# Performance work log

Measured on AMD Instinct MI355X. Metric: run time of the kernel, lower is better.

## Reference

```python
import jax, jax.numpy as jnp
import numpy as np

T, D, FF, E, R = 4096, 1024, 2048, 4, 16
LORA_SCALE = 32.0 / 16.0  # alpha / r


def setup_inputs() -> dict:
    key = jax.random.key(0)
    ks = jax.random.split(key, 12)
    return {
        "x": jax.random.normal(ks[0], (T, D), jnp.float32),
        "gate_w": jax.random.normal(ks[1], (E, D), jnp.float32) * 0.03,
        "gate_up_w": jax.random.normal(ks[2], (D, 2 * FF), jnp.float32)[None].repeat(E, 0) * 0.0
                     + jax.random.normal(ks[2], (E, D, 2 * FF), jnp.float32) * 0.03,
        "gate_up_b": jax.random.normal(ks[3], (E, 2 * FF), jnp.float32) * 0.01,
        "down_w": jax.random.normal(ks[4], (E, FF, D), jnp.float32) * 0.02,
        "down_b": jax.random.normal(ks[5], (E, D), jnp.float32) * 0.01,
        "A_gate": jax.random.normal(ks[6], (E, R, D), jnp.float32) * 0.02,
        "B_gate": jax.random.normal(ks[7], (E, FF, R), jnp.float32) * 0.02,
        "A_up": jax.random.normal(ks[8], (E, R, D), jnp.float32) * 0.02,
        "B_up": jax.random.normal(ks[9], (E, FF, R), jnp.float32) * 0.02,
        "A_down": jax.random.normal(ks[10], (E, R, FF), jnp.float32) * 0.02,
        "B_down": jax.random.normal(ks[11], (E, D, R), jnp.float32) * 0.02,
        "top_k": 2,
    }


def reference(x, gate_w, gate_up_w, gate_up_b, down_w, down_b,
              A_gate, B_gate, A_up, B_up, A_down, B_down, top_k):
    t, d = x.shape
    e = gate_w.shape[0]
    # --- router: logits, softmax (fp32), top-k, renormalize ---
    router_logits = x @ gate_w.T                                   # [T,E]
    rw = jax.nn.softmax(router_logits.astype(jnp.float32), axis=1)
    top_w, sel = jax.lax.top_k(rw, top_k)                          # [T,k]
    top_w = top_w / jnp.sum(top_w, axis=-1, keepdims=True)
    top_w = top_w.astype(x.dtype)
    # dense per-token per-expert combine weights (scatter of top-k weights)
    w = jnp.zeros((t, e), x.dtype).at[jnp.arange(t)[:, None], sel].add(top_w)  # [T,E]
    # --- per-expert SwiGLU MLP with LoRA (vectorized over experts) ---
    gu = jnp.einsum('td,edf->etf', x, gate_up_w) + gate_up_b[:, None, :]       # [E,T,2FF]
    ff = gu.shape[-1] // 2
    gate = gu[..., :ff] + jnp.einsum('td,erd,efr->etf', x, A_gate, B_gate) * LORA_SCALE
    up = gu[..., ff:] + jnp.einsum('td,erd,efr->etf', x, A_up, B_up) * LORA_SCALE
    act = jax.nn.silu(gate) * up                                               # [E,T,FF]
    down = jnp.einsum('etf,efd->etd', act, down_w) + down_b[:, None, :]
    down = down + jnp.einsum('etf,erf,edr->etd', act, A_down, B_down) * LORA_SCALE
    # --- weighted scatter-combine ---
    final = jnp.einsum('etd,te->td', down, w)                                  # [T,D]
    return final, router_logits
```

## Files before the change

kernel.cpp:

```cpp
#include <hip/hip_runtime.h>

#define T_TOK 4096
#define DIM   1024
#define FFD   2048
#define NEXP  4
#define NRP   8704
#define MTILES 68

typedef unsigned short u16;
typedef __attribute__((ext_vector_type(8))) short short8;
typedef __attribute__((ext_vector_type(4))) float f32x4;
typedef __attribute__((ext_vector_type(8))) unsigned short u16x8;
typedef __attribute__((ext_vector_type(4))) unsigned short u16x4;

typedef __attribute__((address_space(1))) unsigned int as1_u32;
typedef __attribute__((address_space(3))) unsigned int as3_u32;

__device__ __forceinline__ u16 f2bf(float f) {
  union { float f; unsigned u; } v; v.f = f;
  unsigned u = v.u;
  return (u16)((u + 0x7fffu + ((u >> 16) & 1u)) >> 16);
}
__device__ __forceinline__ float bf2f(u16 h) {
  union { unsigned u; float f; } v; v.u = ((unsigned)h) << 16;
  return v.f;
}
__device__ __forceinline__ void gload16(const void* g, void* l) {
  __builtin_amdgcn_global_load_lds((const as1_u32*)g, (as3_u32*)l, 16, 0, 0);
}

__global__ void router_k(const float* __restrict__ x, const float* __restrict__ gw,
                         float* __restrict__ logits_out, int* __restrict__ sel,
                         float* __restrict__ selw) {
  int t = blockIdx.x;
  int lane = threadIdx.x;
  float xv[16];
#pragma unroll
  for (int i = 0; i < 16; ++i) xv[i] = x[(size_t)t * DIM + lane + i * 64];
  float l[4];
#pragma unroll
  for (int e = 0; e < 4; ++e) {
    float s = 0.f;
#pragma unroll
    for (int i = 0; i < 16; ++i) s += xv[i] * gw[e * DIM + lane + i * 64];
#pragma unroll
    for (int off = 32; off > 0; off >>= 1) s += __shfl_xor(s, off, 64);
    l[e] = s;
  }
  if (lane == 0) {
#pragma unroll
    for (int e = 0; e < 4; ++e) logits_out[(size_t)t * 4 + e] = l[e];
    int e0 = 0; float b0 = l[0];
    for (int e = 1; e < 4; ++e) if (l[e] > b0) { b0 = l[e]; e0 = e; }
    int e1 = -1; float b1 = -3.4e38f;
    for (int e = 0; e < 4; ++e) if (e != e0 && l[e] > b1) { b1 = l[e]; e1 = e; }
    float p1 = expf(b1 - b0);
    float w0 = 1.f / (1.f + p1);
    sel[2 * t] = e0; sel[2 * t + 1] = e1;
    selw[2 * t] = w0; selw[2 * t + 1] = 1.f - w0;
  }
}

__global__ void scan_k(const int* __restrict__ sel, int* __restrict__ pos,
                       int* __restrict__ offs, int* __restrict__ rowtok,
                       int* __restrict__ pairrow) {
  __shared__ int base[4];
  __shared__ int wsum[16][4];
  __shared__ int off_s[5];
  int tid = threadIdx.x, lane = tid & 63, wid = tid >> 6;
  if (tid < 4) base[tid] = 0;
  __syncthreads();
  for (int chunk = 0; chunk < 4; ++chunk) {
    int t = chunk * 1024 + tid;
    int e0 = sel[2 * t], e1 = sel[2 * t + 1];
    unsigned long long ltm = (1ull << lane) - 1ull;
    bool f[4]; int within[4];
#pragma unroll
    for (int e = 0; e < 4; ++e) {
      f[e] = (e0 == e) || (e1 == e);
      unsigned long long m = __ballot(f[e]);
      within[e] = __popcll(m & ltm);
      if (lane == 0) wsum[wid][e] = __popcll(m);
    }
    __syncthreads();
    int wbase[4] = {0, 0, 0, 0}, tot[4] = {0, 0, 0, 0};
    for (int i = 0; i < 16; ++i)
#pragma unroll
      for (int e = 0; e < 4; ++e) {
        int v = wsum[i][e];
        if (i < wid) wbase[e] += v;
        tot[e] += v;
      }
#pragma unroll
    for (int e = 0; e < 4; ++e)
      if (f[e]) {
        int p = base[e] + wbase[e] + within[e];
        if (e0 == e) pos[2 * t] = p; else pos[2 * t + 1] = p;
      }
    __syncthreads();
    if (tid < 4) base[tid] += tot[tid];
    __syncthreads();
  }
  if (tid == 0) {
    int o = 0;
    for (int e = 0; e < 4; ++e) { off_s[e] = o; o += ((base[e] + 127) >> 7) << 7; }
    off_s[4] = o;
    for (int i = 0; i < 5; ++i) offs[i] = off_s[i];
  }
  __syncthreads();
  for (int r = tid; r < NRP; r += 1024) rowtok[r] = -1;
  __syncthreads();
  for (int t = tid; t < T_TOK; t += 1024) {
#pragma unroll
    for (int s = 0; s < 2; ++s) {
      int e = sel[2 * t + s];
      int rr = off_s[e] + pos[2 * t + s];
      pairrow[2 * t + s] = rr;
      rowtok[rr] = t;
    }
  }
}

__global__ void gather_k(const float* __restrict__ x, const int* __restrict__ rowtok,
                         u16* __restrict__ xg) {
  int r = blockIdx.x, tid = threadIdx.x;
  int t = rowtok[r];
  float4 v = make_float4(0.f, 0.f, 0.f, 0.f);
  if (t >= 0) v = ((const float4*)(x + (size_t)t * DIM))[tid];
  u16x4 o;
  o[0] = f2bf(v.x); o[1] = f2bf(v.y); o[2] = f2bf(v.z); o[3] = f2bf(v.w);
  ((u16x4*)(xg + (size_t)r * DIM))[tid] = o;
}

__global__ void cvtA_k(const float* __restrict__ Ag, const float* __restrict__ Au,
                       const float* __restrict__ Ad, u16* __restrict__ abgu,
                       u16* __restrict__ adb) {
  int g = blockIdx.x * 256 + threadIdx.x;
  if (g < 32768) {
    int flat = g * 4;
    int e = flat >> 15;
    int rem = flat & 32767;
    int q = rem >> 10;
    int d = rem & 1023;
    const float* src = (q < 16) ? (Ag + ((size_t)e * 16 + q) * DIM + d)
                                : (Au + ((size_t)e * 16 + (q - 16)) * DIM + d);
    float4 v = *(const float4*)src;
    u16x4 o; o[0] = f2bf(v.x); o[1] = f2bf(v.y); o[2] = f2bf(v.z); o[3] = f2bf(v.w);
    *(u16x4*)(abgu + (size_t)flat) = o;
  } else {
    int flat = (g - 32768) * 4;
    float4 v = *(const float4*)(Ad + flat);
    u16x4 o; o[0] = f2bf(v.x); o[1] = f2bf(v.y); o[2] = f2bf(v.z); o[3] = f2bf(v.w);
    *(u16x4*)(adb + (size_t)flat) = o;
  }
}

__global__ void xa_k(const u16* __restrict__ xg, const u16* __restrict__ abgu,
                     const int* __restrict__ offs, float* __restrict__ xagu) {
  int r0 = blockIdx.x * 2, lane = threadIdx.x;
  int e = 0;
  if (r0 >= offs[1]) e = 1;
  if (r0 >= offs[2]) e = 2;
  if (r0 >= offs[3]) e = 3;
  float x0[16], x1[16];
#pragma unroll
  for (int i = 0; i < 4; ++i) {
    u16x4 v0 = ((const u16x4*)(xg + (size_t)r0 * DIM))[lane + i * 64];
    u16x4 v1 = ((const u16x4*)(xg + (size_t)(r0 + 1) * DIM))[lane + i * 64];
#pragma unroll
    for (int j = 0; j < 4; ++j) { x0[i * 4 + j] = bf2f(v0[j]); x1[i * 4 + j] = bf2f(v1[j]); }
  }
  const u16* A = abgu + (size_t)e * 32 * DIM;
  for (int q = 0; q < 32; ++q) {
    float s0 = 0.f, s1 = 0.f;
#pragma unroll
    for (int i = 0; i < 4; ++i) {
      u16x4 av = ((const u16x4*)(A + (size_t)q * DIM))[lane + i * 64];
#pragma unroll
      for (int j = 0; j < 4; ++j) {
        float a = bf2f(av[j]);
        s0 += x0[i * 4 + j] * a; s1 += x1[i * 4 + j] * a;
      }
    }
#pragma unroll
    for (int off = 32; off > 0; off >>= 1) { s0 += __shfl_xor(s0, off, 64); s1 += __shfl_xor(s1, off, 64); }
    if (lane == 0) { xagu[(size_t)r0 * 32 + q] = s0; xagu[(size_t)(r0 + 1) * 32 + q] = s1; }
  }
}

__global__ void aad_k(const u16* __restrict__ act, const u16* __restrict__ adb,
                      const int* __restrict__ offs, float* __restrict__ aad) {
  int r0 = blockIdx.x * 2, lane = threadIdx.x;
  int e = 0;
  if (r0 >= offs[1]) e = 1;
  if (r0 >= offs[2]) e = 2;
  if (r0 >= offs[3]) e = 3;
  float x0[32], x1[32];
#pragma unroll
  for (int i = 0; i < 8; ++i) {
    u16x4 v0 = ((const u16x4*)(act + (size_t)r0 * FFD))[lane + i * 64];
    u16x4 v1 = ((const u16x4*)(act + (size_t)(r0 + 1) * FFD))[lane + i * 64];
#pragma unroll
    for (int j = 0; j < 4; ++j) { x0[i * 4 + j] = bf2f(v0[j]); x1[i * 4 + j] = bf2f(v1[j]); }
  }
  const u16* A = adb + (size_t)e * 16 * FFD;
  for (int q = 0; q < 16; ++q) {
    float s0 = 0.f, s1 = 0.f;
#pragma unroll
    for (int i = 0; i < 8; ++i) {
      u16x4 av = ((const u16x4*)(A + (size_t)q * FFD))[lane + i * 64];
#pragma unroll
      for (int j = 0; j < 4; ++j) {
        float a = bf2f(av[j]);
        s0 += x0[i * 4 + j] * a; s1 += x1[i * 4 + j] * a;
      }
    }
#pragma unroll
    for (int off = 32; off > 0; off >>= 1) { s0 += __shfl_xor(s0, off, 64); s1 += __shfl_xor(s1, off, 64); }
    if (lane == 0) { aad[(size_t)r0 * 16 + q] = s0; aad[(size_t)(r0 + 1) * 16 + q] = s1; }
  }
}

__global__ void transpose_k(const float* __restrict__ in, u16* __restrict__ out,
                            int K, int N) {
  int e = blockIdx.z;
  int n0 = blockIdx.x * 32, k0 = blockIdx.y * 32;
  const float* I = in + (size_t)e * K * N;
  u16* O = out + (size_t)e * N * K;
  __shared__ u16 tile[32][33];
#pragma unroll
  for (int i = 0; i < 4; ++i) {
    int k = k0 + threadIdx.y + i * 8;
    tile[threadIdx.y + i * 8][threadIdx.x] = f2bf(I[(size_t)k * N + n0 + threadIdx.x]);
  }
  __syncthreads();
#pragma unroll
  for (int i = 0; i < 4; ++i) {
    int n = n0 + threadIdx.y + i * 8;
    O[(size_t)n * K + k0 + threadIdx.x] = tile[threadIdx.x][threadIdx.y + i * 8];
  }
}

__global__ __launch_bounds__(256) void gemm1_k(
    const u16* __restrict__ xg, const u16* __restrict__ wgu_t,
    const float* __restrict__ gub, const float* __restrict__ Bg,
    const float* __restrict__ Bu, const float* __restrict__ xagu,
    const int* __restrict__ offs, u16* __restrict__ act) {
  __shared__ __align__(16) u16 sAB[24576];
  int tid = threadIdx.x, w = tid >> 6, lane = tid & 63;
  int f0 = blockIdx.x * 64;
  int row0 = blockIdx.y * 128;
  int e = 0;
  if (row0 >= offs[1]) e = 1;
  if (row0 >= offs[2]) e = 2;
  if (row0 >= offs[3]) e = 3;

  int srow = w * 32 + (lane >> 2);
  int scol = ((lane & 3) ^ ((lane >> 3) & 3)) * 8;
  const u16* gA = xg + (size_t)(row0 + srow) * DIM + scol;
  const u16* gA2 = gA + 16 * DIM;
  int n1 = srow, n2 = srow + 16;
  int gr1 = (n1 < 64) ? (f0 + n1) : (2048 + f0 + n1 - 64);
  int gr2 = (n2 < 64) ? (f0 + n2) : (2048 + f0 + n2 - 64);
  const u16* gB1 = wgu_t + ((size_t)e << 22) + (size_t)gr1 * DIM + scol;
  const u16* gB2 = wgu_t + ((size_t)e << 22) + (size_t)gr2 * DIM + scol;
  int fo = (((lane >> 4) ^ ((lane >> 1) & 3))) * 8;
  int ar = (w * 32 + (lane & 15)) * 32 + fo;

  f32x4 acc[2][8];
#pragma unroll
  for (int i = 0; i < 2; ++i)
#pragma unroll
    for (int j = 0; j < 8; ++j) acc[i][j] = f32x4{0.f, 0.f, 0.f, 0.f};

  {
    u16* d0 = sAB + w * 1024;
    gload16(gA, d0); gload16(gA2, d0 + 512);
    gload16(gB1, d0 + 4096); gload16(gB2, d0 + 4608);
    u16* d1 = sAB + 8192 + w * 1024;
    gload16(gA + 32, d1); gload16(gA2 + 32, d1 + 512);
    gload16(gB1 + 32, d1 + 4096); gload16(gB2 + 32, d1 + 4608);
  }
#pragma unroll
  for (int t = 0; t < 32; ++t) {
    if (t == 31) asm volatile("s_waitcnt vmcnt(0)\n\ts_barrier" ::: "memory");
    else         asm volatile("s_waitcnt vmcnt(4)\n\ts_barrier" ::: "memory");
    if (t < 30) {
      int kk = (t + 2) * 32;
      u16* dA = sAB + ((t + 2) % 3) * 8192 + w * 1024;
      gload16(gA + kk, dA); gload16(gA2 + kk, dA + 512);
      gload16(gB1 + kk, dA + 4096); gload16(gB2 + kk, dA + 4608);
    }
    const u16* cA = sAB + (t % 3) * 8192;
    const u16* cB = cA + 4096;
    short8 a[2], bb[8];
#pragma unroll
    for (int mi = 0; mi < 2; ++mi)
      a[mi] = *(const short8*)&cA[ar + mi * 512];
#pragma unroll
    for (int ni = 0; ni < 8; ++ni)
      bb[ni] = *(const short8*)&cB[(ni * 16 + (lane & 15)) * 32 + fo];
#pragma unroll
    for (int mi = 0; mi < 2; ++mi)
#pragma unroll
      for (int ni = 0; ni < 8; ++ni)
        acc[mi][ni] = __builtin_amdgcn_mfma_f32_16x16x32_bf16(a[mi], bb[ni], acc[mi][ni], 0, 0, 0);
  }

  u16* sA = sAB;
  u16* sB = sAB + 4096;
  __syncthreads();
  {
    int r = tid >> 1, kh = tid & 1;
    int sw = (r >> 1) & 3;
    int o0 = r * 32 + ((2 * kh + 0) ^ sw) * 8;
    int o1 = r * 32 + ((2 * kh + 1) ^ sw) * 8;
    u16 tmp[16];
    if (kh == 0) {
#pragma unroll
      for (int q = 0; q < 16; ++q) tmp[q] = f2bf(2.f * xagu[(size_t)(row0 + r) * 32 + q]);
    } else {
#pragma unroll
      for (int q = 0; q < 16; ++q) tmp[q] = 0;
      tmp[0] = 0x3f80;
    }
    *(u16x8*)&sA[o0] = *(u16x8*)&tmp[0];
    *(u16x8*)&sA[o1] = *(u16x8*)&tmp[8];
    int f = (r < 64) ? (f0 + r) : (f0 + r - 64);
    const float* Bsrc = (r < 64) ? Bg : Bu;
    float bias = gub[e * 4096 + ((r < 64) ? f : (2048 + f))];
    if (kh == 0) {
#pragma unroll
      for (int q = 0; q < 16; ++q) tmp[q] = f2bf(Bsrc[((size_t)e * FFD + f) * 16 + q]);
    } else {
#pragma unroll
      for (int q = 0; q < 16; ++q) tmp[q] = 0;
      tmp[0] = f2bf(bias);
    }
    *(u16x8*)&sB[o0] = *(u16x8*)&tmp[0];
    *(u16x8*)&sB[o1] = *(u16x8*)&tmp[8];
  }
  __syncthreads();
  {
    short8 a[2], b[4];
#pragma unroll
    for (int mi = 0; mi < 2; ++mi)
      a[mi] = *(const short8*)&sA[ar + mi * 512];
#pragma unroll
    for (int ni = 0; ni < 4; ++ni)
      b[ni] = *(const short8*)&sB[(ni * 16 + (lane & 15)) * 32 + fo];
#pragma unroll
    for (int mi = 0; mi < 2; ++mi)
#pragma unroll
      for (int ni = 0; ni < 4; ++ni)
        acc[mi][ni] = __builtin_amdgcn_mfma_f32_16x16x32_bf16(a[mi], b[ni], acc[mi][ni], 0, 0, 0);
  }
  __syncthreads();
  {
    int r = tid >> 1, kh = tid & 1;
    int sw = (r >> 1) & 3;
    int o0 = r * 32 + ((2 * kh + 0) ^ sw) * 8;
    int o1 = r * 32 + ((2 * kh + 1) ^ sw) * 8;
    u16 tmp[16];
    if (kh == 0) {
#pragma unroll
      for (int q = 0; q < 16; ++q) tmp[q] = f2bf(2.f * xagu[(size_t)(row0 + r) * 32 + 16 + q]);
    } else {
#pragma unroll
      for (int q = 0; q < 16; ++q) tmp[q] = 0;
      tmp[0] = 0x3f80;
    }
    *(u16x8*)&sA[o0] = *(u16x8*)&tmp[0];
    *(u16x8*)&sA[o1] = *(u16x8*)&tmp[8];
  }
  __syncthreads();
  {
    short8 a[2], b[4];
#pragma unroll
    for (int mi = 0; mi < 2; ++mi)
      a[mi] = *(const short8*)&sA[ar + mi * 512];
#pragma unroll
    for (int ni = 0; ni < 4; ++ni)
      b[ni] = *(const short8*)&sB[((ni + 4) * 16 + (lane & 15)) * 32 + fo];
#pragma unroll
    for (int mi = 0; mi < 2; ++mi)
#pragma unroll
      for (int ni = 0; ni < 4; ++ni)
        acc[mi][ni + 4] = __builtin_amdgcn_mfma_f32_16x16x32_bf16(a[mi], b[ni], acc[mi][ni + 4], 0, 0, 0);
  }
  __syncthreads();
#pragma unroll
  for (int mi = 0; mi < 2; ++mi)
#pragma unroll
    for (int ni = 0; ni < 4; ++ni)
#pragma unroll
      for (int j = 0; j < 4; ++j) {
        int lr = w * 32 + mi * 16 + (lane >> 4) * 4 + j;
        int lc = ni * 16 + (lane & 15);
        float g = acc[mi][ni][j];
        float u = acc[mi][ni + 4][j];
        float s = g / (1.f + __expf(-g));
        sAB[lr * 64 + lc] = f2bf(s * u);
      }
  __syncthreads();
#pragma unroll
  for (int it = 0; it < 4; ++it) {
    int idx = it * 256 + tid;
    int rr = idx >> 3, c8 = (idx & 7) * 8;
    *(u16x8*)(act + (size_t)(row0 + rr) * FFD + f0 + c8) = *(const u16x8*)&sAB[rr * 64 + c8];
  }
}

__global__ __launch_bounds__(256) void gemm2_k(
    const u16* __restrict__ act, const u16* __restrict__ wd_t,
    const float* __restrict__ db, const float* __restrict__ Bd,
    const float* __restrict__ aad, const int* __restrict__ offs,
    u16* __restrict__ down) {
  __shared__ __align__(16) u16 sAB[24576];
  int tid = threadIdx.x, w = tid >> 6, lane = tid & 63;
  int n0 = blockIdx.x * 128;
  int row0 = blockIdx.y * 128;
  int ks = blockIdx.z;
  size_t kbase = (size_t)ks * 1024;
  int e = 0;
  if (row0 >= offs[1]) e = 1;
  if (row0 >= offs[2]) e = 2;
  if (row0 >= offs[3]) e = 3;
  int wm = w >> 1, wn = w & 1;

  int srow = w * 32 + (lane >> 2);
  int scol = ((lane & 3) ^ ((lane >> 3) & 3)) * 8;
  const u16* gA = act + (size_t)(row0 + srow) * FFD + kbase + scol;
  const u16* gA2 = gA + 16 * FFD;
  const u16* gB = wd_t + (size_t)e * DIM * FFD + (size_t)(n0 + srow) * FFD + kbase + scol;
  const u16* gB2 = gB + 16 * FFD;
  int fo = (((lane >> 4) ^ ((lane >> 1) & 3))) * 8;
  int ar = (wm * 64 + (lane & 15)) * 32 + fo;
  int br = (wn * 64 + (lane & 15)) * 32 + fo;

  f32x4 acc[4][4];
#pragma unroll
  for (int i = 0; i < 4; ++i)
#pragma unroll
    for (int j = 0; j < 4; ++j) acc[i][j] = f32x4{0.f, 0.f, 0.f, 0.f};

  {
    u16* d0 = sAB + w * 1024;
    gload16(gA, d0); gload16(gA2, d0 + 512);
    gload16(gB, d0 + 4096); gload16(gB2, d0 + 4608);
    u16* d1 = sAB + 8192 + w * 1024;
    gload16(gA + 32, d1); gload16(gA2 + 32, d1 + 512);
    gload16(gB + 32, d1 + 4096); gload16(gB2 + 32, d1 + 4608);
  }
#pragma unroll
  for (int t = 0; t < 32; ++t) {
    if (t == 31) asm volatile("s_waitcnt vmcnt(0)\n\ts_barrier" ::: "memory");
    else         asm volatile("s_waitcnt vmcnt(4)\n\ts_barrier" ::: "memory");
    if (t < 30) {
      int kk = (t + 2) * 32;
      u16* dA = sAB + ((t + 2) % 3) * 8192 + w * 1024;
      gload16(gA + kk, dA); gload16(gA2 + kk, dA + 512);
      gload16(gB + kk, dA + 4096); gload16(gB2 + kk, dA + 4608);
    }
    const u16* cA = sAB + (t % 3) * 8192;
    const u16* cB = cA + 4096;
    short8 a[4], bb[4];
#pragma unroll
    for (int mi = 0; mi < 4; ++mi)
      a[mi] = *(const short8*)&cA[ar + mi * 512];
#pragma unroll
    for (int ni = 0; ni < 4; ++ni)
      bb[ni] = *(const short8*)&cB[br + ni * 512];
#pragma unroll
    for (int mi = 0; mi < 4; ++mi)
#pragma unroll
      for (int ni = 0; ni < 4; ++ni)
        acc[mi][ni] = __builtin_amdgcn_mfma_f32_16x16x32_bf16(a[mi], bb[ni], acc[mi][ni], 0, 0, 0);
  }

  u16* sA = sAB;
  u16* sB = sAB + 4096;
  if (ks == 0) {
    __syncthreads();
    {
      int r = tid >> 1, kh = tid & 1;
      int sw = (r >> 1) & 3;
      int o0 = r * 32 + ((2 * kh + 0) ^ sw) * 8;
      int o1 = r * 32 + ((2 * kh + 1) ^ sw) * 8;
      u16 tmp[16];
      if (kh == 0) {
#pragma unroll
        for (int q = 0; q < 16; ++q) tmp[q] = f2bf(2.f * aad[(size_t)(row0 + r) * 16 + q]);
      } else {
#pragma unroll
        for (int q = 0; q < 16; ++q) tmp[q] = 0;
        tmp[0] = 0x3f80;
      }
      *(u16x8*)&sA[o0] = *(u16x8*)&tmp[0];
      *(u16x8*)&sA[o1] = *(u16x8*)&tmp[8];
      if (kh == 0) {
#pragma unroll
        for (int q = 0; q < 16; ++q) tmp[q] = f2bf(Bd[((size_t)e * DIM + n0 + r) * 16 + q]);
      } else {
#pragma unroll
        for (int q = 0; q < 16; ++q) tmp[q] = 0;
        tmp[0] = f2bf(db[e * DIM + n0 + r]);
      }
      *(u16x8*)&sB[o0] = *(u16x8*)&tmp[0];
      *(u16x8*)&sB[o1] = *(u16x8*)&tmp[8];
    }
    __syncthreads();
    {
      short8 a[4], b[4];
#pragma unroll
      for (int mi = 0; mi < 4; ++mi)
        a[mi] = *(const short8*)&sA[ar + mi * 512];
#pragma unroll
      for (int ni = 0; ni < 4; ++ni)
        b[ni] = *(const short8*)&sB[br + ni * 512];
#pragma unroll
      for (int mi = 0; mi < 4; ++mi)
#pragma unroll
        for (int ni = 0; ni < 4; ++ni)
          acc[mi][ni] = __builtin_amdgcn_mfma_f32_16x16x32_bf16(a[mi], b[ni], acc[mi][ni], 0, 0, 0);
    }
  }
#pragma unroll
  for (int mi = 0; mi < 4; ++mi)
#pragma unroll
    for (int ni = 0; ni < 4; ++ni)
#pragma unroll
      for (int j = 0; j < 4; ++j) {
        int lr = wm * 64 + mi * 16 + (lane >> 4) * 4 + j;
        int lc = wn * 64 + ni * 16 + (lane & 15);
        down[((size_t)ks * NRP + row0 + lr) * DIM + n0 + lc] = f2bf(acc[mi][ni][j]);
      }
}

__global__ void combine_k(const u16* __restrict__ down, const int* __restrict__ pairrow,
                          const float* __restrict__ selw, float* __restrict__ out) {
  int t = blockIdx.x, tid = threadIdx.x;
  int r0 = pairrow[2 * t], r1 = pairrow[2 * t + 1];
  float w0 = selw[2 * t], w1 = selw[2 * t + 1];
  u16x4 a0 = *(const u16x4*)(down + ((size_t)r0) * DIM + tid * 4);
  u16x4 a1 = *(const u16x4*)(down + ((size_t)NRP + r0) * DIM + tid * 4);
  u16x4 b0 = *(const u16x4*)(down + ((size_t)r1) * DIM + tid * 4);
  u16x4 b1 = *(const u16x4*)(down + ((size_t)NRP + r1) * DIM + tid * 4);
  f32x4 o;
#pragma unroll
  for (int j = 0; j < 4; ++j)
    o[j] = w0 * (bf2f(a0[j]) + bf2f(a1[j])) + w1 * (bf2f(b0[j]) + bf2f(b1[j]));
  *(f32x4*)(out + (size_t)t * DIM + tid * 4) = o;
}

extern "C" void kernel_launch(void* const* d_in, const int* in_sizes, int n_in,
                              void* d_out, int out_size, void* d_ws, size_t ws_size,
                              hipStream_t stream) {
  const float* x         = (const float*)d_in[0];
  const float* gate_w    = (const float*)d_in[1];
  const float* gate_up_w = (const float*)d_in[2];
  const float* gate_up_b = (const float*)d_in[3];
  const float* down_w    = (const float*)d_in[4];
  const float* down_b    = (const float*)d_in[5];
  const float* A_gate    = (const float*)d_in[6];
  const float* B_gate    = (const float*)d_in[7];
  const float* A_up      = (const float*)d_in[8];
  const float* B_up      = (const float*)d_in[9];
  const float* A_down    = (const float*)d_in[10];
  const float* B_down    = (const float*)d_in[11];

  float* out_final  = (float*)d_out;
  float* out_logits = out_final + (size_t)T_TOK * DIM;

  char* ws = (char*)d_ws;
  size_t o = 0;
  auto take = [&](size_t bytes) -> void* {
    void* p = ws + o;
    o = (o + bytes + 255) & ~(size_t)255;
    return p;
  };
  int*   offs    = (int*)take(64);
  int*   sel     = (int*)take((size_t)T_TOK * 2 * 4);
  float* selw    = (float*)take((size_t)T_TOK * 2 * 4);
  int*   pos     = (int*)take((size_t)T_TOK * 2 * 4);
  int*   pairrow = (int*)take((size_t)T_TOK * 2 * 4);
  int*   rowtok  = (int*)take((size_t)NRP * 4);
  float* xagu    = (float*)take((size_t)NRP * 32 * 4);
  float* aadb    = (float*)take((size_t)NRP * 16 * 4);
  u16*   abgu    = (u16*)take((size_t)NEXP * 32 * DIM * 2);
  u16*   adb     = (u16*)take((size_t)NEXP * 16 * FFD * 2);
  u16*   xg      = (u16*)take((size_t)NRP * DIM * 2);
  u16*   actb    = (u16*)take((size_t)NRP * FFD * 2);
  u16*   downb   = (u16*)take((size_t)2 * NRP * DIM * 2);
  u16*   wgu_t   = (u16*)take((size_t)NEXP * 2 * FFD * DIM * 2);
  u16*   wd_t    = (u16*)take((size_t)NEXP * DIM * FFD * 2);
  (void)ws_size; (void)in_sizes; (void)n_in; (void)out_size;

  transpose_k<<<dim3(128, 32, NEXP), dim3(32, 8), 0, stream>>>(gate_up_w, wgu_t, DIM, 2 * FFD);
  transpose_k<<<dim3(32, 64, NEXP), dim3(32, 8), 0, stream>>>(down_w, wd_t, FFD, DIM);
  cvtA_k<<<256, 256, 0, stream>>>(A_gate, A_up, A_down, abgu, adb);

  router_k<<<T_TOK, 64, 0, stream>>>(x, gate_w, out_logits, sel, selw);
  scan_k<<<1, 1024, 0, stream>>>(sel, pos, offs, rowtok, pairrow);
  gather_k<<<NRP, 256, 0, stream>>>(x, rowtok, xg);
  xa_k<<<NRP / 2, 64, 0, stream>>>(xg, abgu, offs, xagu);
  gemm1_k<<<dim3(32, MTILES), 256, 0, stream>>>(xg, wgu_t, gate_up_b, B_gate, B_up,
                                                xagu, offs, actb);
  aad_k<<<NRP / 2, 64, 0, stream>>>(actb, adb, offs, aadb);
  gemm2_k<<<dim3(8, MTILES, 2), 256, 0, stream>>>(actb, wd_t, down_b, B_down, aadb, offs, downb);
  combine_k<<<T_TOK, 256, 0, stream>>>(downb, pairrow, selw, out_final);
}
```

Baseline: 272.4 us.

## Enlarge GEMM output tiles to 128x256 and restructure SwiGLU epilogue through LDS

```diff
diff --git a/kernel.cpp b/kernel.cpp
--- a/kernel.cpp
+++ b/kernel.cpp
@@ -241,184 +241,159 @@
   }
 }
 
-__global__ __launch_bounds__(256) void gemm1_k(
+__global__ __launch_bounds__(256, 2) void gemm1_k(
     const u16* __restrict__ xg, const u16* __restrict__ wgu_t,
     const float* __restrict__ gub, const float* __restrict__ Bg,
     const float* __restrict__ Bu, const float* __restrict__ xagu,
     const int* __restrict__ offs, u16* __restrict__ act) {
-  __shared__ __align__(16) u16 sAB[24576];
+  __shared__ __align__(16) u16 sAB[36864];
   int tid = threadIdx.x, w = tid >> 6, lane = tid & 63;
-  int f0 = blockIdx.x * 64;
+  int f0 = blockIdx.x * 128;
   int row0 = blockIdx.y * 128;
   int e = 0;
   if (row0 >= offs[1]) e = 1;
   if (row0 >= offs[2]) e = 2;
   if (row0 >= offs[3]) e = 3;
-
-  int srow = w * 32 + (lane >> 2);
+  int wm = w >> 1, wn = w & 1;
+
+  int srow = lane >> 2;
   int scol = ((lane & 3) ^ ((lane >> 3) & 3)) * 8;
-  const u16* gA = xg + (size_t)(row0 + srow) * DIM + scol;
-  const u16* gA2 = gA + 16 * DIM;
-  int n1 = srow, n2 = srow + 16;
-  int gr1 = (n1 < 64) ? (f0 + n1) : (2048 + f0 + n1 - 64);
-  int gr2 = (n2 < 64) ? (f0 + n2) : (2048 + f0 + n2 - 64);
-  const u16* gB1 = wgu_t + ((size_t)e << 22) + (size_t)gr1 * DIM + scol;
-  const u16* gB2 = wgu_t + ((size_t)e << 22) + (size_t)gr2 * DIM + scol;
+  const u16* gA = xg + (size_t)(row0 + w * 32 + srow) * DIM + scol;
+  int bhalf = (w < 2) ? (f0 + w * 64) : (2048 + f0 + (w - 2) * 64);
+  const u16* gB = wgu_t + ((size_t)e << 22) + (size_t)(bhalf + srow) * DIM + scol;
   int fo = (((lane >> 4) ^ ((lane >> 1) & 3))) * 8;
-  int ar = (w * 32 + (lane & 15)) * 32 + fo;
-
-  f32x4 acc[2][8];
-#pragma unroll
-  for (int i = 0; i < 2; ++i)
+  int arb = (wm * 64 + (lane & 15)) * 32 + fo;
+  int brb = 4096 + (wn * 128 + (lane & 15)) * 32 + fo;
+
+  f32x4 acc[4][8];
+#pragma unroll
+  for (int i = 0; i < 4; ++i)
 #pragma unroll
     for (int j = 0; j < 8; ++j) acc[i][j] = f32x4{0.f, 0.f, 0.f, 0.f};
 
-  {
-    u16* d0 = sAB + w * 1024;
-    gload16(gA, d0); gload16(gA2, d0 + 512);
-    gload16(gB1, d0 + 4096); gload16(gB2, d0 + 4608);
-    u16* d1 = sAB + 8192 + w * 1024;
-    gload16(gA + 32, d1); gload16(gA2 + 32, d1 + 512);
-    gload16(gB1 + 32, d1 + 4096); gload16(gB2 + 32, d1 + 4608);
+#pragma unroll
+  for (int p = 0; p < 2; ++p) {
+    u16* dA = sAB + p * 12288 + w * 1024;
+    gload16(gA + p * 32, dA); gload16(gA + 16 * DIM + p * 32, dA + 512);
+    u16* dB = sAB + p * 12288 + 4096 + w * 2048;
+    gload16(gB + p * 32, dB); gload16(gB + 16 * DIM + p * 32, dB + 512);
+    gload16(gB + 32 * DIM + p * 32, dB + 1024); gload16(gB + 48 * DIM + p * 32, dB + 1536);
   }
 #pragma unroll
   for (int t = 0; t < 32; ++t) {
     if (t == 31) asm volatile("s_waitcnt vmcnt(0)\n\ts_barrier" ::: "memory");
-    else         asm volatile("s_waitcnt vmcnt(4)\n\ts_barrier" ::: "memory");
+    else         asm volatile("s_waitcnt vmcnt(6)\n\ts_barrier" ::: "memory");
     if (t < 30) {
       int kk = (t + 2) * 32;
-      u16* dA = sAB + ((t + 2) % 3) * 8192 + w * 1024;
-      gload16(gA + kk, dA); gload16(gA2 + kk, dA + 512);
-      gload16(gB1 + kk, dA + 4096); gload16(gB2 + kk, dA + 4608);
-    }
-    const u16* cA = sAB + (t % 3) * 8192;
-    const u16* cB = cA + 4096;
-    short8 a[2], bb[8];
-#pragma unroll
-    for (int mi = 0; mi < 2; ++mi)
-      a[mi] = *(const short8*)&cA[ar + mi * 512];
+      int bo = ((t + 2) % 3) * 12288;
+      u16* dA = sAB + bo + w * 1024;
+      gload16(gA + kk, dA); gload16(gA + 16 * DIM + kk, dA + 512);
+      u16* dB = sAB + bo + 4096 + w * 2048;
+      gload16(gB + kk, dB); gload16(gB + 16 * DIM + kk, dB + 512);
+      gload16(gB + 32 * DIM + kk, dB + 1024); gload16(gB + 48 * DIM + kk, dB + 1536);
+    }
+    const u16* cb = sAB + (t % 3) * 12288;
+    short8 a[4], bb[8];
+#pragma unroll
+    for (int mi = 0; mi < 4; ++mi)
+      a[mi] = *(const short8*)&cb[arb + mi * 512];
 #pragma unroll
     for (int ni = 0; ni < 8; ++ni)
-      bb[ni] = *(const short8*)&cB[(ni * 16 + (lane & 15)) * 32 + fo];
-#pragma unroll
-    for (int mi = 0; mi < 2; ++mi)
+      bb[ni] = *(const short8*)&cb[brb + ni * 512];
+#pragma unroll
+    for (int mi = 0; mi < 4; ++mi)
 #pragma unroll
       for (int ni = 0; ni < 8; ++ni)
         acc[mi][ni] = __builtin_amdgcn_mfma_f32_16x16x32_bf16(a[mi], bb[ni], acc[mi][ni], 0, 0, 0);
   }
 
-  u16* sA = sAB;
-  u16* sB = sAB + 4096;
   __syncthreads();
   {
-    int r = tid >> 1, kh = tid & 1;
-    int sw = (r >> 1) & 3;
-    int o0 = r * 32 + ((2 * kh + 0) ^ sw) * 8;
-    int o1 = r * 32 + ((2 * kh + 1) ^ sw) * 8;
+    int rl = tid & 127, half = tid >> 7;
+    int sw = (rl >> 1) & 3;
+    int abase = half * 12288 + rl * 32;
     u16 tmp[16];
-    if (kh == 0) {
-#pragma unroll
-      for (int q = 0; q < 16; ++q) tmp[q] = f2bf(2.f * xagu[(size_t)(row0 + r) * 32 + q]);
-    } else {
-#pragma unroll
-      for (int q = 0; q < 16; ++q) tmp[q] = 0;
-      tmp[0] = 0x3f80;
-    }
-    *(u16x8*)&sA[o0] = *(u16x8*)&tmp[0];
-    *(u16x8*)&sA[o1] = *(u16x8*)&tmp[8];
-    int f = (r < 64) ? (f0 + r) : (f0 + r - 64);
-    const float* Bsrc = (r < 64) ? Bg : Bu;
-    float bias = gub[e * 4096 + ((r < 64) ? f : (2048 + f))];
-    if (kh == 0) {
-#pragma unroll
-      for (int q = 0; q < 16; ++q) tmp[q] = f2bf(Bsrc[((size_t)e * FFD + f) * 16 + q]);
-    } else {
-#pragma unroll
-      for (int q = 0; q < 16; ++q) tmp[q] = 0;
-      tmp[0] = f2bf(bias);
-    }
-    *(u16x8*)&sB[o0] = *(u16x8*)&tmp[0];
-    *(u16x8*)&sB[o1] = *(u16x8*)&tmp[8];
+#pragma unroll
+    for (int q = 0; q < 16; ++q) tmp[q] = f2bf(2.f * xagu[(size_t)(row0 + rl) * 32 + half * 16 + q]);
+    *(u16x8*)&sAB[abase + (0 ^ sw) * 8] = *(u16x8*)&tmp[0];
+    *(u16x8*)&sAB[abase + (1 ^ sw) * 8] = *(u16x8*)&tmp[8];
+    u16 t2[8] = {0x3f80, 0, 0, 0, 0, 0, 0, 0};
+    u16 t3[8] = {0, 0, 0, 0, 0, 0, 0, 0};
+    *(u16x8*)&sAB[abase + (2 ^ sw) * 8] = *(u16x8*)&t2[0];
+    *(u16x8*)&sAB[abase + (3 ^ sw) * 8] = *(u16x8*)&t3[0];
+    int r = tid, fb = r & 127, bh = r >> 7;
+    int swb = (r >> 1) & 3;
+    int bbase = 4096 + r * 32;
+    const float* Bsrc = bh ? Bu : Bg;
+    float bias = gub[e * 4096 + (bh ? (2048 + f0 + fb) : (f0 + fb))];
+    u16 tb[16];
+#pragma unroll
+    for (int q = 0; q < 16; ++q) tb[q] = f2bf(Bsrc[((size_t)e * FFD + f0 + fb) * 16 + q]);
+    *(u16x8*)&sAB[bbase + (0 ^ swb) * 8] = *(u16x8*)&tb[0];
+    *(u16x8*)&sAB[bbase + (1 ^ swb) * 8] = *(u16x8*)&tb[8];
+    u16 t2b[8] = {f2bf(bias), 0, 0, 0, 0, 0, 0, 0};
+    *(u16x8*)&sAB[bbase + (2 ^ swb) * 8] = *(u16x8*)&t2b[0];
+    *(u16x8*)&sAB[bbase + (3 ^ swb) * 8] = *(u16x8*)&t3[0];
   }
   __syncthreads();
   {
-    short8 a[2], b[4];
-#pragma unroll
-    for (int mi = 0; mi < 2; ++mi)
-      a[mi] = *(const short8*)&sA[ar + mi * 512];
-#pragma unroll
-    for (int ni = 0; ni < 4; ++ni)
-      b[ni] = *(const short8*)&sB[(ni * 16 + (lane & 15)) * 32 + fo];
-#pragma unroll
-    for (int mi = 0; mi < 2; ++mi)
-#pragma unroll
-      for (int ni = 0; ni < 4; ++ni)
-        acc[mi][ni] = __builtin_amdgcn_mfma_f32_16x16x32_bf16(a[mi], b[ni], acc[mi][ni], 0, 0, 0);
-  }
+    int aBase = wn ? 12288 : 0;
+    short8 a[4], bb[8];
+#pragma unroll
+    for (int mi = 0; mi < 4; ++mi)
+      a[mi] = *(const short8*)&sAB[aBase + arb + mi * 512];
+#pragma unroll
+    for (int ni = 0; ni < 8; ++ni)
+      bb[ni] = *(const short8*)&sAB[brb + ni * 512];
+#pragma unroll
+    for (int mi = 0; mi < 4; ++mi)
+#pragma unroll
+      for (int ni = 0; ni < 8; ++ni)
+        acc[mi][ni] = __builtin_amdgcn_mfma_f32_16x16x32_bf16(a[mi], bb[ni], acc[mi][ni], 0, 0, 0);
+  }
+  __syncthreads();
+#pragma unroll
+  for (int mi = 0; mi < 4; ++mi)
+#pragma unroll
+    for (int ni = 0; ni < 8; ++ni)
+#pragma unroll
+      for (int j = 0; j < 4; ++j) {
+        int row = wm * 64 + mi * 16 + (lane >> 4) * 4 + j;
+        int br = wn * 128 + ni * 16 + (lane & 15);
+        int key = ((row & 3) ^ ((row >> 2) & 3)) << 4;
+        sAB[row * 256 + (br ^ key)] = f2bf(acc[mi][ni][j]);
+      }
   __syncthreads();
   {
-    int r = tid >> 1, kh = tid & 1;
-    int sw = (r >> 1) & 3;
-    int o0 = r * 32 + ((2 * kh + 0) ^ sw) * 8;
-    int o1 = r * 32 + ((2 * kh + 1) ^ sw) * 8;
-    u16 tmp[16];
-    if (kh == 0) {
-#pragma unroll
-      for (int q = 0; q < 16; ++q) tmp[q] = f2bf(2.f * xagu[(size_t)(row0 + r) * 32 + 16 + q]);
-    } else {
-#pragma unroll
-      for (int q = 0; q < 16; ++q) tmp[q] = 0;
-      tmp[0] = 0x3f80;
-    }
-    *(u16x8*)&sA[o0] = *(u16x8*)&tmp[0];
-    *(u16x8*)&sA[o1] = *(u16x8*)&tmp[8];
-  }
-  __syncthreads();
-  {
-    short8 a[2], b[4];
-#pragma unroll
-    for (int mi = 0; mi < 2; ++mi)
-      a[mi] = *(const short8*)&sA[ar + mi * 512];
-#pragma unroll
-    for (int ni = 0; ni < 4; ++ni)
-      b[ni] = *(const short8*)&sB[((ni + 4) * 16 + (lane & 15)) * 32 + fo];
-#pragma unroll
-    for (int mi = 0; mi < 2; ++mi)
-#pragma unroll
-      for (int ni = 0; ni < 4; ++ni)
-        acc[mi][ni + 4] = __builtin_amdgcn_mfma_f32_16x16x32_bf16(a[mi], b[ni], acc[mi][ni + 4], 0, 0, 0);
-  }
-  __syncthreads();
-#pragma unroll
-  for (int mi = 0; mi < 2; ++mi)
-#pragma unroll
-    for (int ni = 0; ni < 4; ++ni)
-#pragma unroll
-      for (int j = 0; j < 4; ++j) {
-        int lr = w * 32 + mi * 16 + (lane >> 4) * 4 + j;
-        int lc = ni * 16 + (lane & 15);
-        float g = acc[mi][ni][j];
-        float u = acc[mi][ni + 4][j];
+    int fc = (tid & 15) * 8;
+    int rb = tid >> 4;
+#pragma unroll
+    for (int it = 0; it < 8; ++it) {
+      int row = rb + it * 16;
+      int key = ((row & 3) ^ ((row >> 2) & 3)) << 4;
+      u16x8 gv = *(const u16x8*)&sAB[row * 256 + (fc ^ key)];
+      u16x8 uv = *(const u16x8*)&sAB[row * 256 + 128 + (fc ^ key)];
+      u16x8 ov;
+#pragma unroll
+      for (int j = 0; j < 8; ++j) {
+        float g = bf2f(gv[j]);
+        float u = bf2f(uv[j]);
         float s = g / (1.f + __expf(-g));
-        sAB[lr * 64 + lc] = f2bf(s * u);
-      }
-  __syncthreads();
-#pragma unroll
-  for (int it = 0; it < 4; ++it) {
-    int idx = it * 256 + tid;
-    int rr = idx >> 3, c8 = (idx & 7) * 8;
-    *(u16x8*)(act + (size_t)(row0 + rr) * FFD + f0 + c8) = *(const u16x8*)&sAB[rr * 64 + c8];
-  }
-}
-
-__global__ __launch_bounds__(256) void gemm2_k(
+        ov[j] = f2bf(s * u);
+      }
+      *(u16x8*)(act + (size_t)(row0 + row) * FFD + f0 + fc) = ov;
+    }
+  }
+}
+
+__global__ __launch_bounds__(256, 2) void gemm2_k(
     const u16* __restrict__ act, const u16* __restrict__ wd_t,
     const float* __restrict__ db, const float* __restrict__ Bd,
     const float* __restrict__ aad, const int* __restrict__ offs,
     u16* __restrict__ down) {
-  __shared__ __align__(16) u16 sAB[24576];
+  __shared__ __align__(16) u16 sAB[36864];
   int tid = threadIdx.x, w = tid >> 6, lane = tid & 63;
-  int n0 = blockIdx.x * 128;
+  int n0 = blockIdx.x * 256;
   int row0 = blockIdx.y * 128;
   int ks = blockIdx.z;
   size_t kbase = (size_t)ks * 1024;
@@ -428,58 +403,56 @@
   if (row0 >= offs[3]) e = 3;
   int wm = w >> 1, wn = w & 1;
 
-  int srow = w * 32 + (lane >> 2);
+  int srow = lane >> 2;
   int scol = ((lane & 3) ^ ((lane >> 3) & 3)) * 8;
-  const u16* gA = act + (size_t)(row0 + srow) * FFD + kbase + scol;
-  const u16* gA2 = gA + 16 * FFD;
-  const u16* gB = wd_t + (size_t)e * DIM * FFD + (size_t)(n0 + srow) * FFD + kbase + scol;
-  const u16* gB2 = gB + 16 * FFD;
+  const u16* gA = act + (size_t)(row0 + w * 32 + srow) * FFD + kbase + scol;
+  const u16* gB = wd_t + (size_t)e * DIM * FFD + (size_t)(n0 + w * 64 + srow) * FFD + kbase + scol;
   int fo = (((lane >> 4) ^ ((lane >> 1) & 3))) * 8;
-  int ar = (wm * 64 + (lane & 15)) * 32 + fo;
-  int br = (wn * 64 + (lane & 15)) * 32 + fo;
-
-  f32x4 acc[4][4];
+  int arb = (wm * 64 + (lane & 15)) * 32 + fo;
+  int brb = 4096 + (wn * 128 + (lane & 15)) * 32 + fo;
+
+  f32x4 acc[4][8];
 #pragma unroll
   for (int i = 0; i < 4; ++i)
 #pragma unroll
-    for (int j = 0; j < 4; ++j) acc[i][j] = f32x4{0.f, 0.f, 0.f, 0.f};
-
-  {
-    u16* d0 = sAB + w * 1024;
-    gload16(gA, d0); gload16(gA2, d0 + 512);
-    gload16(gB, d0 + 4096); gload16(gB2, d0 + 4608);
-    u16* d1 = sAB + 8192 + w * 1024;
-    gload16(gA + 32, d1); gload16(gA2 + 32, d1 + 512);
-    gload16(gB + 32, d1 + 4096); gload16(gB2 + 32, d1 + 4608);
+    for (int j = 0; j < 8; ++j) acc[i][j] = f32x4{0.f, 0.f, 0.f, 0.f};
+
+#pragma unroll
+  for (int p = 0; p < 2; ++p) {
+    u16* dA = sAB + p * 12288 + w * 1024;
+    gload16(gA + p * 32, dA); gload16(gA + 16 * FFD + p * 32, dA + 512);
+    u16* dB = sAB + p * 12288 + 4096 + w * 2048;
+    gload16(gB + p * 32, dB); gload16(gB + 16 * FFD + p * 32, dB + 512);
+    gload16(gB + 32 * FFD + p * 32, dB + 1024); gload16(gB + 48 * FFD + p * 32, dB + 1536);
   }
 #pragma unroll
   for (int t = 0; t < 32; ++t) {
     if (t == 31) asm volatile("s_waitcnt vmcnt(0)\n\ts_barrier" ::: "memory");
-    else         asm volatile("s_waitcnt vmcnt(4)\n\ts_barrier" ::: "memory");
+    else         asm volatile("s_waitcnt vmcnt(6)\n\ts_barrier" ::: "memory");
     if (t < 30) {
       int kk = (t + 2) * 32;
-      u16* dA = sAB + ((t + 2) % 3) * 8192 + w * 1024;
-      gload16(gA + kk, dA); gload16(gA2 + kk, dA + 512);
-      gload16(gB + kk, dA + 4096); gload16(gB2 + kk, dA + 4608);
-    }
-    const u16* cA = sAB + (t % 3) * 8192;
-    const u16* cB = cA + 4096;
-    short8 a[4], bb[4];
+      int bo = ((t + 2) % 3) * 12288;
+      u16* dA = sAB + bo + w * 1024;
+      gload16(gA + kk, dA); gload16(gA + 16 * FFD + kk, dA + 512);
+      u16* dB = sAB + bo + 4096 + w * 2048;
+      gload16(gB + kk, dB); gload16(gB + 16 * FFD + kk, dB + 512);
+      gload16(gB + 32 * FFD + kk, dB + 1024); gload16(gB + 48 * FFD + kk, dB + 1536);
+    }
+    const u16* cb = sAB + (t % 3) * 12288;
+    short8 a[4], bb[8];
 #pragma unroll
     for (int mi = 0; mi < 4; ++mi)
-      a[mi] = *(const short8*)&cA[ar + mi * 512];
-#pragma unroll
-    for (int ni = 0; ni < 4; ++ni)
-      bb[ni] = *(const short8*)&cB[br + ni * 512];
+      a[mi] = *(const short8*)&cb[arb + mi * 512];
+#pragma unroll
+    for (int ni = 0; ni < 8; ++ni)
+      bb[ni] = *(const short8*)&cb[brb + ni * 512];
 #pragma unroll
     for (int mi = 0; mi < 4; ++mi)
 #pragma unroll
-      for (int ni = 0; ni < 4; ++ni)
+      for (int ni = 0; ni < 8; ++ni)
         acc[mi][ni] = __builtin_amdgcn_mfma_f32_16x16x32_bf16(a[mi], bb[ni], acc[mi][ni], 0, 0, 0);
   }
 
-  u16* sA = sAB;
-  u16* sB = sAB + 4096;
   if (ks == 0) {
     __syncthreads();
     {
@@ -496,43 +469,45 @@
         for (int q = 0; q < 16; ++q) tmp[q] = 0;
         tmp[0] = 0x3f80;
       }
-      *(u16x8*)&sA[o0] = *(u16x8*)&tmp[0];
-      *(u16x8*)&sA[o1] = *(u16x8*)&tmp[8];
-      if (kh == 0) {
-#pragma unroll
-        for (int q = 0; q < 16; ++q) tmp[q] = f2bf(Bd[((size_t)e * DIM + n0 + r) * 16 + q]);
-      } else {
-#pragma unroll
-        for (int q = 0; q < 16; ++q) tmp[q] = 0;
-        tmp[0] = f2bf(db[e * DIM + n0 + r]);
-      }
-      *(u16x8*)&sB[o0] = *(u16x8*)&tmp[0];
-      *(u16x8*)&sB[o1] = *(u16x8*)&tmp[8];
+      *(u16x8*)&sAB[o0] = *(u16x8*)&tmp[0];
+      *(u16x8*)&sAB[o1] = *(u16x8*)&tmp[8];
+      int r2 = tid;
+      int swb = (r2 >> 1) & 3;
+      int bbase = 4096 + r2 * 32;
+      u16 tb[16];
+#pragma unroll
+      for (int q = 0; q < 16; ++q) tb[q] = f2bf(Bd[((size_t)e * DIM + n0 + r2) * 16 + q]);
+      *(u16x8*)&sAB[bbase + (0 ^ swb) * 8] = *(u16x8*)&tb[0];
+      *(u16x8*)&sAB[bbase + (1 ^ swb) * 8] = *(u16x8*)&tb[8];
+      u16 t2b[8] = {f2bf(db[e * DIM + n0 + r2]), 0, 0, 0, 0, 0, 0, 0};
+      u16 t3b[8] = {0, 0, 0, 0, 0, 0, 0, 0};
+      *(u16x8*)&sAB[bbase + (2 ^ swb) * 8] = *(u16x8*)&t2b[0];
+      *(u16x8*)&sAB[bbase + (3 ^ swb) * 8] = *(u16x8*)&t3b[0];
     }
     __syncthreads();
     {
-      short8 a[4], b[4];
+      short8 a[4], bb[8];
 #pragma unroll
       for (int mi = 0; mi < 4; ++mi)
-        a[mi] = *(const short8*)&sA[ar + mi * 512];
-#pragma unroll
-      for (int ni = 0; ni < 4; ++ni)
-        b[ni] = *(const short8*)&sB[br + ni * 512];
+        a[mi] = *(const short8*)&sAB[arb + mi * 512];
+#pragma unroll
+      for (int ni = 0; ni < 8; ++ni)
+        bb[ni] = *(const short8*)&sAB[brb + ni * 512];
 #pragma unroll
       for (int mi = 0; mi < 4; ++mi)
 #pragma unroll
-        for (int ni = 0; ni < 4; ++ni)
-          acc[mi][ni] = __builtin_amdgcn_mfma_f32_16x16x32_bf16(a[mi], b[ni], acc[mi][ni], 0, 0, 0);
+        for (int ni = 0; ni < 8; ++ni)
+          acc[mi][ni] = __builtin_amdgcn_mfma_f32_16x16x32_bf16(a[mi], bb[ni], acc[mi][ni], 0, 0, 0);
     }
   }
 #pragma unroll
   for (int mi = 0; mi < 4; ++mi)
 #pragma unroll
-    for (int ni = 0; ni < 4; ++ni)
+    for (int ni = 0; ni < 8; ++ni)
 #pragma unroll
       for (int j = 0; j < 4; ++j) {
         int lr = wm * 64 + mi * 16 + (lane >> 4) * 4 + j;
-        int lc = wn * 64 + ni * 16 + (lane & 15);
+        int lc = wn * 128 + ni * 16 + (lane & 15);
         down[((size_t)ks * NRP + row0 + lr) * DIM + n0 + lc] = f2bf(acc[mi][ni][j]);
       }
 }
@@ -604,9 +579,9 @@
   scan_k<<<1, 1024, 0, stream>>>(sel, pos, offs, rowtok, pairrow);
   gather_k<<<NRP, 256, 0, stream>>>(x, rowtok, xg);
   xa_k<<<NRP / 2, 64, 0, stream>>>(xg, abgu, offs, xagu);
-  gemm1_k<<<dim3(32, MTILES), 256, 0, stream>>>(xg, wgu_t, gate_up_b, B_gate, B_up,
+  gemm1_k<<<dim3(16, MTILES), 256, 0, stream>>>(xg, wgu_t, gate_up_b, B_gate, B_up,
                                                 xagu, offs, actb);
   aad_k<<<NRP / 2, 64, 0, stream>>>(actb, adb, offs, aadb);
-  gemm2_k<<<dim3(8, MTILES, 2), 256, 0, stream>>>(actb, wd_t, down_b, B_down, aadb, offs, downb);
+  gemm2_k<<<dim3(4, MTILES, 2), 256, 0, stream>>>(actb, wd_t, down_b, B_down, aadb, offs, downb);
   combine_k<<<T_TOK, 256, 0, stream>>>(downb, pairrow, selw, out_final);
 }
```

Result: faster. 260.0 us (-4.6%).
